# Optimization experiments

Measured on AMD Instinct MI355X. Metric: run time of the kernel, lower is better.

The kernel has to match this reference:

```python
import jax, jax.numpy as jnp
import numpy as np
import math

B, S, H, NH = 8, 1024, 768, 12
DH = H // NH  # 64
EPS = 1e-5


def layernorm(x, gamma, beta):
    mu = jnp.mean(x, axis=-1, keepdims=True)
    var = jnp.mean(jnp.square(x - mu), axis=-1, keepdims=True)
    return (x - mu) * jax.lax.rsqrt(var + EPS) * gamma + beta


def setup_inputs() -> dict:
    key = jax.random.key(0)
    ks = jax.random.split(key, 12)
    sc = 1.0 / math.sqrt(H)
    return {
        "x1": jax.random.normal(ks[0], (B, S, H), jnp.float32),
        "weight_mask": jax.random.uniform(ks[1], (B, 1, S, S), jnp.float32),
        "Wq": jax.random.normal(ks[2], (H, H), jnp.float32) * sc,
        "bq": jnp.zeros((H,), jnp.float32),
        "Wk": jax.random.normal(ks[3], (H, H), jnp.float32) * sc,
        "bk": jnp.zeros((H,), jnp.float32),
        "Wv": jax.random.normal(ks[4], (H, H), jnp.float32) * sc,
        "bv": jnp.zeros((H,), jnp.float32),
        "g1": jnp.ones((H,), jnp.float32),
        "be1": jnp.zeros((H,), jnp.float32),
        "g2": jnp.ones((H,), jnp.float32),
        "be2": jnp.zeros((H,), jnp.float32),
        "W1": jax.random.normal(ks[5], (H, 2 * H), jnp.float32) * sc,
        "b1": jnp.zeros((2 * H,), jnp.float32),
        "W2": jax.random.normal(ks[6], (2 * H, H), jnp.float32) * (1.0 / math.sqrt(2 * H)),
        "b2": jnp.zeros((H,), jnp.float32),
    }


def reference(x1, weight_mask, Wq, bq, Wk, bk, Wv, bv, g1, be1, g2, be2, W1, b1, W2, b2):
    # QKV projections [B,S,H]
    q_mixed = x1 @ Wq + bq
    k_mixed = x1 @ Wk + bk
    v_mixed = x1 @ Wv + bv

    def heads(t):  # [B,S,H] -> [B,NH,S,DH]
        return t.reshape(B, S, NH, DH).transpose(0, 2, 1, 3)

    q, k, v = heads(q_mixed), heads(k_mixed), heads(v_mixed)
    scores = jnp.einsum("bhqd,bhkd->bhqk", q, k) / math.sqrt(DH)
    probs = jax.nn.softmax(scores, axis=-1)
    probs = probs * weight_mask  # post-softmax elementwise mask
    ctx = jnp.einsum("bhqk,bhkd->bhqd", probs, v)
    ctx = ctx.transpose(0, 2, 1, 3).reshape(B, S, H)

    # residual uses the mixed query (as in the original code); dropout = eval identity
    x = layernorm(ctx + q_mixed, g1, be1)
    ff = jnp.maximum(x @ W1 + b1, 0.0) @ W2 + b2
    out = layernorm(x + ff, g2, be2)
    return out
```

## Files before the change

kernel.cpp:

```cpp
#include <hip/hip_runtime.h>
#include <math.h>

#define Bsz 8
#define Sq  1024
#define Hd  768
#define NHd 12
#define DHd 64
#define QS  2304

typedef __attribute__((ext_vector_type(8))) short bf16x8;
typedef __attribute__((ext_vector_type(4))) float f32x4;

__device__ __forceinline__ ushort f2bf(float f) {
    unsigned u = __float_as_uint(f);
    u += 0x7fffu + ((u >> 16) & 1u);
    return (ushort)(u >> 16);
}
__device__ __forceinline__ float bf2f(ushort u) {
    return __uint_as_float(((unsigned)u) << 16);
}
__device__ __forceinline__ void load_lds16(const ushort* g, ushort* l) {
    __builtin_amdgcn_global_load_lds((const __attribute__((address_space(1))) void*)g,
                                     (__attribute__((address_space(3))) void*)l, 16, 0, 0);
}

__global__ __launch_bounds__(256) void cvt_bf16(const float* __restrict__ a,
                                                ushort* __restrict__ o, int n4) {
    int i = blockIdx.x * 256 + threadIdx.x;
    if (i < n4) {
        float4 f = ((const float4*)a)[i];
        ushort4 u;
        u.x = f2bf(f.x); u.y = f2bf(f.y); u.z = f2bf(f.z); u.w = f2bf(f.w);
        ((ushort4*)o)[i] = u;
    }
}

__global__ __launch_bounds__(256) void transpose_cvt(const float* __restrict__ in,
                                                     ushort* __restrict__ out,
                                                     int K, int N) {
    __shared__ float tile[32][33];
    const int n0 = blockIdx.x * 32, k0 = blockIdx.y * 32;
    const int tx = threadIdx.x & 31, ty = threadIdx.x >> 5;
#pragma unroll
    for (int i = ty; i < 32; i += 8)
        tile[i][tx] = in[(size_t)(k0 + i) * N + n0 + tx];
    __syncthreads();
#pragma unroll
    for (int i = ty; i < 32; i += 8)
        out[(size_t)(n0 + i) * K + k0 + tx] = f2bf(tile[tx][i]);
}

__global__ __launch_bounds__(256) void concat_bias(const float* __restrict__ bq,
                                                   const float* __restrict__ bk,
                                                   const float* __restrict__ bv,
                                                   float* __restrict__ o) {
    int i = blockIdx.x * 256 + threadIdx.x;
    if (i < 2304)
        o[i] = i < 768 ? bq[i] : (i < 1536 ? bk[i - 768] : bv[i - 1536]);
}

template<bool RELU, bool OUT_BF16>
__global__ __launch_bounds__(256) void gemm_mfma(const ushort* __restrict__ A,
                                                 const ushort* __restrict__ BT,
                                                 const float* __restrict__ bias,
                                                 void* __restrict__ Cout,
                                                 int M, int N, int K) {
    const int bm = blockIdx.y * 128;
    const int bn = blockIdx.x * 128;
    const int t  = threadIdx.x;
    const int wave = t >> 6, lane = t & 63;
    const int l15 = lane & 15, quad = lane >> 4;
    const int wm = (wave >> 1) * 64, wn = (wave & 1) * 64;

    __shared__ ushort As[128 * 64];
    __shared__ ushort Bs[128 * 64];

    f32x4 acc[4][4];
#pragma unroll
    for (int i = 0; i < 4; ++i)
#pragma unroll
        for (int j = 0; j < 4; ++j) acc[i][j] = (f32x4){0, 0, 0, 0};

    const int g_row[4] = {(0 * 256 + t) >> 3, (1 * 256 + t) >> 3, (2 * 256 + t) >> 3, (3 * 256 + t) >> 3};
    const int g_pc     = t & 7;

    for (int k0 = 0; k0 < K; k0 += 64) {
#pragma unroll
        for (int it = 0; it < 4; ++it) {
            const int row = g_row[it];
            const int cb  = g_pc ^ (row & 7);
            load_lds16(A  + (size_t)(bm + row) * K + k0 + cb * 8,
                       As + (size_t)(it * 256 + wave * 64) * 8);
            load_lds16(BT + (size_t)(bn + row) * K + k0 + cb * 8,
                       Bs + (size_t)(it * 256 + wave * 64) * 8);
        }
        __syncthreads();
#pragma unroll
        for (int kk = 0; kk < 64; kk += 32) {
            bf16x8 af[4], bfr[4];
            const int cbk = (kk >> 3) + quad;
#pragma unroll
            for (int i = 0; i < 4; ++i) {
                const int rowA = wm + i * 16 + l15;
                af[i]  = *(const bf16x8*)(As + (size_t)(rowA * 8 + (cbk ^ (rowA & 7))) * 8);
                const int rowB = wn + i * 16 + l15;
                bfr[i] = *(const bf16x8*)(Bs + (size_t)(rowB * 8 + (cbk ^ (rowB & 7))) * 8);
            }
#pragma unroll
            for (int i = 0; i < 4; ++i)
#pragma unroll
                for (int j = 0; j < 4; ++j)
                    acc[i][j] = __builtin_amdgcn_mfma_f32_16x16x32_bf16(af[i], bfr[j], acc[i][j], 0, 0, 0);
        }
        __syncthreads();
    }

#pragma unroll
    for (int i = 0; i < 4; ++i) {
#pragma unroll
        for (int r = 0; r < 4; ++r) {
            const int m = bm + wm + i * 16 + quad * 4 + r;
#pragma unroll
            for (int j = 0; j < 4; ++j) {
                const int n = bn + wn + j * 16 + l15;
                float v = acc[i][j][r] + bias[n];
                if (RELU) v = fmaxf(v, 0.0f);
                if (OUT_BF16) ((ushort*)Cout)[(size_t)m * N + n] = f2bf(v);
                else          ((float*)Cout)[(size_t)m * N + n] = v;
            }
        }
    }
}

__global__ __launch_bounds__(256) void attn_mfma(const ushort* __restrict__ qkv,
                                                 const float* __restrict__ mask,
                                                 float* __restrict__ ctx) {
    const int nqt  = Sq / 64;
    const int bh   = blockIdx.x / nqt;
    const int qt   = blockIdx.x % nqt;
    const int b    = bh / NHd;
    const int h    = bh % NHd;
    const int t    = threadIdx.x;
    const int wave = t >> 6;
    const int lane = t & 63;
    const int l15  = lane & 15;
    const int quad = lane >> 4;

    __shared__ ushort Qs[64][72];
    __shared__ ushort Ks[64][72];
    __shared__ ushort Vt[DHd][72];
    __shared__ ushort Pt[4][16][72];

    const size_t rowbase = (size_t)b * Sq;
    const size_t colbase = (size_t)h * DHd;

    {
        const int r = t >> 2, c = (t & 3) * 16;
        const ushort* src = qkv + (rowbase + qt * 64 + r) * QS + colbase + c;
        *(int4*)&Qs[r][c]     = *(const int4*)(src);
        *(int4*)&Qs[r][c + 8] = *(const int4*)(src + 8);
    }
    __syncthreads();

    bf16x8 qf0 = *(const bf16x8*)&Qs[wave * 16 + l15][quad * 8];
    bf16x8 qf1 = *(const bf16x8*)&Qs[wave * 16 + l15][32 + quad * 8];

    f32x4 o[4] = {{0,0,0,0},{0,0,0,0},{0,0,0,0},{0,0,0,0}};
    float m_i[4] = {-INFINITY, -INFINITY, -INFINITY, -INFINITY};
    float l_i[4] = {0, 0, 0, 0};

    for (int k0 = 0; k0 < Sq; k0 += 64) {
        {
            const int r = t >> 2, c = (t & 3) * 16;
            const ushort* src = qkv + (rowbase + k0 + r) * QS + 768 + colbase + c;
            int4 ka = *(const int4*)(src);
            int4 kc = *(const int4*)(src + 8);
            *(int4*)&Ks[r][c]     = ka;
            *(int4*)&Ks[r][c + 8] = kc;

            const int kp = t & 31, db = (t >> 5) * 8;
            union { int4 v; ushort u[8]; } v0, v1;
            v0.v = *(const int4*)(qkv + (rowbase + k0 + 2 * kp)     * QS + 1536 + colbase + db);
            v1.v = *(const int4*)(qkv + (rowbase + k0 + 2 * kp + 1) * QS + 1536 + colbase + db);
#pragma unroll
            for (int j = 0; j < 8; ++j)
                *(unsigned*)&Vt[db + j][2 * kp] = (unsigned)v0.u[j] | ((unsigned)v1.u[j] << 16);
        }
        __syncthreads();

        float mv[4][4];
        const int qrow0 = qt * 64 + wave * 16 + quad * 4;
#pragma unroll
        for (int nt = 0; nt < 4; ++nt) {
            const int kcol = k0 + nt * 16 + l15;
#pragma unroll
            for (int r = 0; r < 4; ++r)
                mv[nt][r] = mask[((size_t)b * Sq + (qrow0 + r)) * Sq + kcol];
        }

        f32x4 s[4] = {{0,0,0,0},{0,0,0,0},{0,0,0,0},{0,0,0,0}};
#pragma unroll
        for (int nt = 0; nt < 4; ++nt) {
            bf16x8 b0 = *(const bf16x8*)&Ks[nt * 16 + l15][quad * 8];
            bf16x8 b1 = *(const bf16x8*)&Ks[nt * 16 + l15][32 + quad * 8];
            s[nt] = __builtin_amdgcn_mfma_f32_16x16x32_bf16(qf0, b0, s[nt], 0, 0, 0);
            s[nt] = __builtin_amdgcn_mfma_f32_16x16x32_bf16(qf1, b1, s[nt], 0, 0, 0);
        }
#pragma unroll
        for (int nt = 0; nt < 4; ++nt)
#pragma unroll
            for (int r = 0; r < 4; ++r) s[nt][r] *= 0.125f;

        float mnew[4], alpha[4], rs[4];
#pragma unroll
        for (int r = 0; r < 4; ++r) {
            float mx = fmaxf(fmaxf(s[0][r], s[1][r]), fmaxf(s[2][r], s[3][r]));
#pragma unroll
            for (int off = 1; off < 16; off <<= 1) mx = fmaxf(mx, __shfl_xor(mx, off));
            mnew[r]  = fmaxf(m_i[r], mx);
            alpha[r] = __expf(m_i[r] - mnew[r]);
            m_i[r]   = mnew[r];
        }
        float p[4][4];
#pragma unroll
        for (int r = 0; r < 4; ++r) rs[r] = 0.0f;
#pragma unroll
        for (int nt = 0; nt < 4; ++nt)
#pragma unroll
            for (int r = 0; r < 4; ++r) {
                p[nt][r] = __expf(s[nt][r] - mnew[r]);
                rs[r] += p[nt][r];
            }
#pragma unroll
        for (int r = 0; r < 4; ++r) {
#pragma unroll
            for (int off = 1; off < 16; off <<= 1) rs[r] += __shfl_xor(rs[r], off);
            l_i[r] = l_i[r] * alpha[r] + rs[r];
        }
#pragma unroll
        for (int dt = 0; dt < 4; ++dt)
#pragma unroll
            for (int r = 0; r < 4; ++r) o[dt][r] *= alpha[r];

#pragma unroll
        for (int nt = 0; nt < 4; ++nt)
#pragma unroll
            for (int r = 0; r < 4; ++r)
                *(ushort*)&Pt[wave][quad * 4 + r][nt * 16 + l15] = f2bf(p[nt][r] * mv[nt][r]);

#pragma unroll
        for (int st = 0; st < 2; ++st) {
            bf16x8 pf = *(const bf16x8*)&Pt[wave][l15][st * 32 + quad * 8];
#pragma unroll
            for (int dt = 0; dt < 4; ++dt) {
                bf16x8 vf = *(const bf16x8*)&Vt[dt * 16 + l15][st * 32 + quad * 8];
                o[dt] = __builtin_amdgcn_mfma_f32_16x16x32_bf16(pf, vf, o[dt], 0, 0, 0);
            }
        }
        __syncthreads();
    }

#pragma unroll
    for (int r = 0; r < 4; ++r) {
        const float inv = 1.0f / l_i[r];
        const size_t row = rowbase + qt * 64 + wave * 16 + quad * 4 + r;
#pragma unroll
        for (int dt = 0; dt < 4; ++dt)
            ctx[row * Hd + colbase + dt * 16 + l15] = o[dt][r] * inv;
    }
}

template<bool RES_BF16, bool EMIT_BF16>
__global__ __launch_bounds__(256) void ln_fused(const float* __restrict__ a,
                                                const void* __restrict__ res, int res_stride,
                                                const float* __restrict__ g,
                                                const float* __restrict__ be,
                                                float* __restrict__ outf,
                                                ushort* __restrict__ outb) {
    const int row = blockIdx.x;
    const int t   = threadIdx.x;
    const float* pa = a + (size_t)row * Hd;
    __shared__ float red[4];
    float v[3];
#pragma unroll
    for (int i = 0; i < 3; ++i) {
        const int idx = t + i * 256;
        float rv;
        if (RES_BF16) rv = bf2f(((const ushort*)res)[(size_t)row * res_stride + idx]);
        else          rv = ((const float*)res)[(size_t)row * res_stride + idx];
        v[i] = pa[idx] + rv;
    }

    float s = v[0] + v[1] + v[2];
#pragma unroll
    for (int off = 32; off > 0; off >>= 1) s += __shfl_xor(s, off);
    if ((t & 63) == 0) red[t >> 6] = s;
    __syncthreads();
    const float mu = (red[0] + red[1] + red[2] + red[3]) * (1.0f / Hd);
    __syncthreads();

    float sq = 0.0f;
#pragma unroll
    for (int i = 0; i < 3; ++i) {
        v[i] -= mu;
        sq = fmaf(v[i], v[i], sq);
    }
#pragma unroll
    for (int off = 32; off > 0; off >>= 1) sq += __shfl_xor(sq, off);
    if ((t & 63) == 0) red[t >> 6] = sq;
    __syncthreads();
    const float var = (red[0] + red[1] + red[2] + red[3]) * (1.0f / Hd);
    const float rs  = rsqrtf(var + 1e-5f);
#pragma unroll
    for (int i = 0; i < 3; ++i) {
        const int idx = t + i * 256;
        const float o = v[i] * rs * g[idx] + be[idx];
        outf[(size_t)row * Hd + idx] = o;
        if (EMIT_BF16) outb[(size_t)row * Hd + idx] = f2bf(o);
    }
}

extern "C" void kernel_launch(void* const* d_in, const int* in_sizes, int n_in,
                              void* d_out, int out_size, void* d_ws, size_t ws_size,
                              hipStream_t stream) {
    const float* x1    = (const float*)d_in[0];
    const float* wmask = (const float*)d_in[1];
    const float* Wq    = (const float*)d_in[2];
    const float* bq    = (const float*)d_in[3];
    const float* Wk    = (const float*)d_in[4];
    const float* bk    = (const float*)d_in[5];
    const float* Wv    = (const float*)d_in[6];
    const float* bv    = (const float*)d_in[7];
    const float* g1    = (const float*)d_in[8];
    const float* be1   = (const float*)d_in[9];
    const float* g2    = (const float*)d_in[10];
    const float* be2   = (const float*)d_in[11];
    const float* W1    = (const float*)d_in[12];
    const float* b1    = (const float*)d_in[13];
    const float* W2    = (const float*)d_in[14];
    const float* b2    = (const float*)d_in[15];
    float* out = (float*)d_out;

    const size_t NT = (size_t)Bsz * Sq * Hd;
    const int M = Bsz * Sq;

    char* p = (char*)d_ws;
    ushort* xb     = (ushort*)p;  p += NT * 2;
    ushort* WqkvT  = (ushort*)p;  p += (size_t)2304 * 768 * 2;
    ushort* W1T    = (ushort*)p;  p += (size_t)1536 * 768 * 2;
    ushort* W2T    = (ushort*)p;  p += (size_t)768 * 1536 * 2;
    float*  qkvbias= (float*)p;   p += 2304 * 4 + 256;
    ushort* qkvb   = (ushort*)p;  p += (size_t)M * QS * 2;
    float*  ctxb   = (float*)p;   p += NT * 4;
    float*  xf     = (float*)p;   p += NT * 4;
    ushort* xbf    = (ushort*)p;  p += NT * 2;
    ushort* hb     = qkvb;
    float*  ffb    = ctxb;

    dim3 blk(256);

    cvt_bf16<<<dim3((int)(NT / 4 / 256)), blk, 0, stream>>>(x1, xb, (int)(NT / 4));

    transpose_cvt<<<dim3(24, 24), blk, 0, stream>>>(Wq, WqkvT,                 768, 768);
    transpose_cvt<<<dim3(24, 24), blk, 0, stream>>>(Wk, WqkvT + 768 * 768,     768, 768);
    transpose_cvt<<<dim3(24, 24), blk, 0, stream>>>(Wv, WqkvT + 2 * 768 * 768, 768, 768);
    transpose_cvt<<<dim3(48, 24), blk, 0, stream>>>(W1, W1T, 768, 1536);
    transpose_cvt<<<dim3(24, 48), blk, 0, stream>>>(W2, W2T, 1536, 768);
    concat_bias<<<dim3(9), blk, 0, stream>>>(bq, bk, bv, qkvbias);

    gemm_mfma<false, true><<<dim3(2304 / 128, M / 128), blk, 0, stream>>>(
        xb, WqkvT, qkvbias, qkvb, M, 2304, 768);

    attn_mfma<<<dim3(Bsz * NHd * (Sq / 64)), blk, 0, stream>>>(qkvb, wmask, ctxb);

    ln_fused<true, true><<<dim3(M), blk, 0, stream>>>(ctxb, qkvb, QS, g1, be1, xf, xbf);

    gemm_mfma<true, true><<<dim3(1536 / 128, M / 128), blk, 0, stream>>>(
        xbf, W1T, b1, hb, M, 1536, 768);

    gemm_mfma<false, false><<<dim3(768 / 128, M / 128), blk, 0, stream>>>(
        hb, W2T, b2, ffb, M, 768, 1536);

    ln_fused<false, false><<<dim3(M), blk, 0, stream>>>(xf, ffb, Hd, g2, be2, out, nullptr);
}
```

Measured before the change: 402.2 us.

## Restructure attention with 32x32 MFMA tiles, folded scale and no running max

Rewrites the attention kernel so each block handles 128 query rows using 32x32x16 bf16 MFMA. Q and K fragments are loaded straight from global memory into registers instead of staging through LDS, and the transposed V tile is double-buffered in LDS. The 1/sqrt(DH) scale is folded into the Wk weights and bk bias during preprocessing. The online-softmax running max and per-tile rescaling are dropped: exp(score) is taken directly and the row sum is reduced once at the end. This cuts per-tile work and synchronisation, but removes overflow protection, so correctness relies on scores staying in a small range.

```diff
diff --git a/kernel.cpp b/kernel.cpp
--- a/kernel.cpp
+++ b/kernel.cpp
@@ -10,6 +10,7 @@
 
 typedef __attribute__((ext_vector_type(8))) short bf16x8;
 typedef __attribute__((ext_vector_type(4))) float f32x4;
+typedef __attribute__((ext_vector_type(16))) float f32x16;
 
 __device__ __forceinline__ ushort f2bf(float f) {
     unsigned u = __float_as_uint(f);
@@ -37,13 +38,13 @@
 
 __global__ __launch_bounds__(256) void transpose_cvt(const float* __restrict__ in,
                                                      ushort* __restrict__ out,
-                                                     int K, int N) {
+                                                     int K, int N, float scale) {
     __shared__ float tile[32][33];
     const int n0 = blockIdx.x * 32, k0 = blockIdx.y * 32;
     const int tx = threadIdx.x & 31, ty = threadIdx.x >> 5;
 #pragma unroll
     for (int i = ty; i < 32; i += 8)
-        tile[i][tx] = in[(size_t)(k0 + i) * N + n0 + tx];
+        tile[i][tx] = in[(size_t)(k0 + i) * N + n0 + tx] * scale;
     __syncthreads();
 #pragma unroll
     for (int i = ty; i < 32; i += 8)
@@ -56,7 +57,7 @@
                                                    float* __restrict__ o) {
     int i = blockIdx.x * 256 + threadIdx.x;
     if (i < 2304)
-        o[i] = i < 768 ? bq[i] : (i < 1536 ? bk[i - 768] : bv[i - 1536]);
+        o[i] = i < 768 ? bq[i] : (i < 1536 ? bk[i - 768] * 0.125f : bv[i - 1536]);
 }
 
 template<bool RELU, bool OUT_BF16>
@@ -132,141 +133,118 @@
     }
 }
 
-__global__ __launch_bounds__(256) void attn_mfma(const ushort* __restrict__ qkv,
-                                                 const float* __restrict__ mask,
-                                                 float* __restrict__ ctx) {
-    const int nqt  = Sq / 64;
-    const int bh   = blockIdx.x / nqt;
-    const int qt   = blockIdx.x % nqt;
-    const int b    = bh / NHd;
-    const int h    = bh % NHd;
-    const int t    = threadIdx.x;
-    const int wave = t >> 6;
-    const int lane = t & 63;
-    const int l15  = lane & 15;
-    const int quad = lane >> 4;
-
-    __shared__ ushort Qs[64][72];
-    __shared__ ushort Ks[64][72];
-    __shared__ ushort Vt[DHd][72];
-    __shared__ ushort Pt[4][16][72];
+__global__ __launch_bounds__(256, 3) void attn_mfma(const ushort* __restrict__ qkv,
+                                                    const float* __restrict__ mask,
+                                                    float* __restrict__ ctx) {
+    const int nqt = Sq / 128;
+    const int bh  = blockIdx.x / nqt;
+    const int qt  = blockIdx.x % nqt;
+    const int b   = bh / NHd;
+    const int h   = bh % NHd;
+    const int t   = threadIdx.x;
+    const int wave = t >> 6, lane = t & 63;
+    const int l31 = lane & 31, half = lane >> 5;
+
+    __shared__ ushort Vt[2][64][72];
+    __shared__ ushort Pt[4][32][72];
 
     const size_t rowbase = (size_t)b * Sq;
-    const size_t colbase = (size_t)h * DHd;
-
+    const int q0 = qt * 128 + wave * 32;
+
+    bf16x8 qf[4];
     {
-        const int r = t >> 2, c = (t & 3) * 16;
-        const ushort* src = qkv + (rowbase + qt * 64 + r) * QS + colbase + c;
-        *(int4*)&Qs[r][c]     = *(const int4*)(src);
-        *(int4*)&Qs[r][c + 8] = *(const int4*)(src + 8);
-    }
-    __syncthreads();
-
-    bf16x8 qf0 = *(const bf16x8*)&Qs[wave * 16 + l15][quad * 8];
-    bf16x8 qf1 = *(const bf16x8*)&Qs[wave * 16 + l15][32 + quad * 8];
-
-    f32x4 o[4] = {{0,0,0,0},{0,0,0,0},{0,0,0,0},{0,0,0,0}};
-    float m_i[4] = {-INFINITY, -INFINITY, -INFINITY, -INFINITY};
-    float l_i[4] = {0, 0, 0, 0};
-
-    for (int k0 = 0; k0 < Sq; k0 += 64) {
+        const ushort* qrow = qkv + (rowbase + q0 + l31) * QS + h * DHd + half * 8;
+#pragma unroll
+        for (int ds = 0; ds < 4; ++ds) qf[ds] = *(const bf16x8*)(qrow + ds * 16);
+    }
+
+    const int kp = t & 31, db = (t >> 5) * 8;
+
+    {
+        const ushort* vp = qkv + (rowbase + 2 * kp) * QS + 1536 + h * DHd + db;
+        union { int4 v; ushort u[8]; } a, c;
+        a.v = *(const int4*)vp;
+        c.v = *(const int4*)(vp + QS);
+#pragma unroll
+        for (int j = 0; j < 8; ++j)
+            *(unsigned*)&Vt[0][db + j][2 * kp] = (unsigned)a.u[j] | ((unsigned)c.u[j] << 16);
+    }
+    __syncthreads();
+
+    f32x16 o0, o1;
+    float rs[16];
+#pragma unroll
+    for (int r = 0; r < 16; ++r) { o0[r] = 0.0f; o1[r] = 0.0f; rs[r] = 0.0f; }
+
+    for (int kt = 0; kt < 16; ++kt) {
+        const int k0  = kt * 64;
+        const int cur = kt & 1;
+
+        if (kt < 15) {
+            const ushort* vp = qkv + (rowbase + k0 + 64 + 2 * kp) * QS + 1536 + h * DHd + db;
+            union { int4 v; ushort u[8]; } a, c;
+            a.v = *(const int4*)vp;
+            c.v = *(const int4*)(vp + QS);
+#pragma unroll
+            for (int j = 0; j < 8; ++j)
+                *(unsigned*)&Vt[cur ^ 1][db + j][2 * kp] = (unsigned)a.u[j] | ((unsigned)c.u[j] << 16);
+        }
+
+        bf16x8 kf0[4], kf1[4];
         {
-            const int r = t >> 2, c = (t & 3) * 16;
-            const ushort* src = qkv + (rowbase + k0 + r) * QS + 768 + colbase + c;
-            int4 ka = *(const int4*)(src);
-            int4 kc = *(const int4*)(src + 8);
-            *(int4*)&Ks[r][c]     = ka;
-            *(int4*)&Ks[r][c + 8] = kc;
-
-            const int kp = t & 31, db = (t >> 5) * 8;
-            union { int4 v; ushort u[8]; } v0, v1;
-            v0.v = *(const int4*)(qkv + (rowbase + k0 + 2 * kp)     * QS + 1536 + colbase + db);
-            v1.v = *(const int4*)(qkv + (rowbase + k0 + 2 * kp + 1) * QS + 1536 + colbase + db);
-#pragma unroll
-            for (int j = 0; j < 8; ++j)
-                *(unsigned*)&Vt[db + j][2 * kp] = (unsigned)v0.u[j] | ((unsigned)v1.u[j] << 16);
+            const ushort* kr0 = qkv + (rowbase + k0 + l31) * QS + Hd + h * DHd + half * 8;
+            const ushort* kr1 = kr0 + 32 * QS;
+#pragma unroll
+            for (int ds = 0; ds < 4; ++ds) {
+                kf0[ds] = *(const bf16x8*)(kr0 + ds * 16);
+                kf1[ds] = *(const bf16x8*)(kr1 + ds * 16);
+            }
+        }
+
+        f32x16 s0, s1;
+#pragma unroll
+        for (int r = 0; r < 16; ++r) { s0[r] = 0.0f; s1[r] = 0.0f; }
+#pragma unroll
+        for (int ds = 0; ds < 4; ++ds) {
+            s0 = __builtin_amdgcn_mfma_f32_32x32x16_bf16(qf[ds], kf0[ds], s0, 0, 0, 0);
+            s1 = __builtin_amdgcn_mfma_f32_32x32x16_bf16(qf[ds], kf1[ds], s1, 0, 0, 0);
+        }
+
+        const float* mrow = mask + ((size_t)b * Sq + q0) * Sq + k0;
+#pragma unroll
+        for (int r = 0; r < 16; ++r) {
+            const int row = (r & 3) + 8 * (r >> 2) + 4 * half;
+            const float e0 = __expf(s0[r]);
+            const float e1 = __expf(s1[r]);
+            rs[r] += e0 + e1;
+            const float m0 = mrow[(size_t)row * Sq + l31];
+            const float m1 = mrow[(size_t)row * Sq + 32 + l31];
+            Pt[wave][row][l31]      = f2bf(e0 * m0);
+            Pt[wave][row][32 + l31] = f2bf(e1 * m1);
+        }
+
+#pragma unroll
+        for (int ks = 0; ks < 4; ++ks) {
+            bf16x8 pf = *(const bf16x8*)&Pt[wave][l31][ks * 16 + half * 8];
+            bf16x8 va = *(const bf16x8*)&Vt[cur][l31][ks * 16 + half * 8];
+            bf16x8 vb = *(const bf16x8*)&Vt[cur][32 + l31][ks * 16 + half * 8];
+            o0 = __builtin_amdgcn_mfma_f32_32x32x16_bf16(pf, va, o0, 0, 0, 0);
+            o1 = __builtin_amdgcn_mfma_f32_32x32x16_bf16(pf, vb, o1, 0, 0, 0);
         }
         __syncthreads();
-
-        float mv[4][4];
-        const int qrow0 = qt * 64 + wave * 16 + quad * 4;
-#pragma unroll
-        for (int nt = 0; nt < 4; ++nt) {
-            const int kcol = k0 + nt * 16 + l15;
-#pragma unroll
-            for (int r = 0; r < 4; ++r)
-                mv[nt][r] = mask[((size_t)b * Sq + (qrow0 + r)) * Sq + kcol];
-        }
-
-        f32x4 s[4] = {{0,0,0,0},{0,0,0,0},{0,0,0,0},{0,0,0,0}};
-#pragma unroll
-        for (int nt = 0; nt < 4; ++nt) {
-            bf16x8 b0 = *(const bf16x8*)&Ks[nt * 16 + l15][quad * 8];
-            bf16x8 b1 = *(const bf16x8*)&Ks[nt * 16 + l15][32 + quad * 8];
-            s[nt] = __builtin_amdgcn_mfma_f32_16x16x32_bf16(qf0, b0, s[nt], 0, 0, 0);
-            s[nt] = __builtin_amdgcn_mfma_f32_16x16x32_bf16(qf1, b1, s[nt], 0, 0, 0);
-        }
-#pragma unroll
-        for (int nt = 0; nt < 4; ++nt)
-#pragma unroll
-            for (int r = 0; r < 4; ++r) s[nt][r] *= 0.125f;
-
-        float mnew[4], alpha[4], rs[4];
-#pragma unroll
-        for (int r = 0; r < 4; ++r) {
-            float mx = fmaxf(fmaxf(s[0][r], s[1][r]), fmaxf(s[2][r], s[3][r]));
-#pragma unroll
-            for (int off = 1; off < 16; off <<= 1) mx = fmaxf(mx, __shfl_xor(mx, off));
-            mnew[r]  = fmaxf(m_i[r], mx);
-            alpha[r] = __expf(m_i[r] - mnew[r]);
-            m_i[r]   = mnew[r];
-        }
-        float p[4][4];
-#pragma unroll
-        for (int r = 0; r < 4; ++r) rs[r] = 0.0f;
-#pragma unroll
-        for (int nt = 0; nt < 4; ++nt)
-#pragma unroll
-            for (int r = 0; r < 4; ++r) {
-                p[nt][r] = __expf(s[nt][r] - mnew[r]);
-                rs[r] += p[nt][r];
-            }
-#pragma unroll
-        for (int r = 0; r < 4; ++r) {
-#pragma unroll
-            for (int off = 1; off < 16; off <<= 1) rs[r] += __shfl_xor(rs[r], off);
-            l_i[r] = l_i[r] * alpha[r] + rs[r];
-        }
-#pragma unroll
-        for (int dt = 0; dt < 4; ++dt)
-#pragma unroll
-            for (int r = 0; r < 4; ++r) o[dt][r] *= alpha[r];
-
-#pragma unroll
-        for (int nt = 0; nt < 4; ++nt)
-#pragma unroll
-            for (int r = 0; r < 4; ++r)
-                *(ushort*)&Pt[wave][quad * 4 + r][nt * 16 + l15] = f2bf(p[nt][r] * mv[nt][r]);
-
-#pragma unroll
-        for (int st = 0; st < 2; ++st) {
-            bf16x8 pf = *(const bf16x8*)&Pt[wave][l15][st * 32 + quad * 8];
-#pragma unroll
-            for (int dt = 0; dt < 4; ++dt) {
-                bf16x8 vf = *(const bf16x8*)&Vt[dt * 16 + l15][st * 32 + quad * 8];
-                o[dt] = __builtin_amdgcn_mfma_f32_16x16x32_bf16(pf, vf, o[dt], 0, 0, 0);
-            }
-        }
-        __syncthreads();
-    }
-
-#pragma unroll
-    for (int r = 0; r < 4; ++r) {
-        const float inv = 1.0f / l_i[r];
-        const size_t row = rowbase + qt * 64 + wave * 16 + quad * 4 + r;
-#pragma unroll
-        for (int dt = 0; dt < 4; ++dt)
-            ctx[row * Hd + colbase + dt * 16 + l15] = o[dt][r] * inv;
+    }
+
+#pragma unroll
+    for (int r = 0; r < 16; ++r) {
+#pragma unroll
+        for (int off = 1; off < 32; off <<= 1) rs[r] += __shfl_xor(rs[r], off);
+    }
+#pragma unroll
+    for (int r = 0; r < 16; ++r) {
+        const float inv = 1.0f / rs[r];
+        const size_t row = rowbase + q0 + (r & 3) + 8 * (r >> 2) + 4 * half;
+        ctx[row * Hd + h * DHd + l31]      = o0[r] * inv;
+        ctx[row * Hd + h * DHd + 32 + l31] = o1[r] * inv;
     }
 }
 
@@ -310,11 +288,11 @@
     if ((t & 63) == 0) red[t >> 6] = sq;
     __syncthreads();
     const float var = (red[0] + red[1] + red[2] + red[3]) * (1.0f / Hd);
-    const float rs  = rsqrtf(var + 1e-5f);
+    const float rsq = rsqrtf(var + 1e-5f);
 #pragma unroll
     for (int i = 0; i < 3; ++i) {
         const int idx = t + i * 256;
-        const float o = v[i] * rs * g[idx] + be[idx];
+        const float o = v[i] * rsq * g[idx] + be[idx];
         outf[(size_t)row * Hd + idx] = o;
         if (EMIT_BF16) outb[(size_t)row * Hd + idx] = f2bf(o);
     }
@@ -361,17 +339,17 @@
 
     cvt_bf16<<<dim3((int)(NT / 4 / 256)), blk, 0, stream>>>(x1, xb, (int)(NT / 4));
 
-    transpose_cvt<<<dim3(24, 24), blk, 0, stream>>>(Wq, WqkvT,                 768, 768);
-    transpose_cvt<<<dim3(24, 24), blk, 0, stream>>>(Wk, WqkvT + 768 * 768,     768, 768);
-    transpose_cvt<<<dim3(24, 24), blk, 0, stream>>>(Wv, WqkvT + 2 * 768 * 768, 768, 768);
-    transpose_cvt<<<dim3(48, 24), blk, 0, stream>>>(W1, W1T, 768, 1536);
-    transpose_cvt<<<dim3(24, 48), blk, 0, stream>>>(W2, W2T, 1536, 768);
+    transpose_cvt<<<dim3(24, 24), blk, 0, stream>>>(Wq, WqkvT,                 768, 768, 1.0f);
+    transpose_cvt<<<dim3(24, 24), blk, 0, stream>>>(Wk, WqkvT + 768 * 768,     768, 768, 0.125f);
+    transpose_cvt<<<dim3(24, 24), blk, 0, stream>>>(Wv, WqkvT + 2 * 768 * 768, 768, 768, 1.0f);
+    transpose_cvt<<<dim3(48, 24), blk, 0, stream>>>(W1, W1T, 768, 1536, 1.0f);
+    transpose_cvt<<<dim3(24, 48), blk, 0, stream>>>(W2, W2T, 1536, 768, 1.0f);
     concat_bias<<<dim3(9), blk, 0, stream>>>(bq, bk, bv, qkvbias);
 
     gemm_mfma<false, true><<<dim3(2304 / 128, M / 128), blk, 0, stream>>>(
         xb, WqkvT, qkvbias, qkvb, M, 2304, 768);
 
-    attn_mfma<<<dim3(Bsz * NHd * (Sq / 64)), blk, 0, stream>>>(qkvb, wmask, ctxb);
+    attn_mfma<<<dim3(Bsz * NHd * (Sq / 128)), blk, 0, stream>>>(qkvb, wmask, ctxb);
 
     ln_fused<true, true><<<dim3(M), blk, 0, stream>>>(ctxb, qkvb, QS, g1, be1, xf, xbf);
 
```

New measurement: 455.9 us. 13.4% more time.
